# Kernel tuning notes

Hardware: AMD Instinct MI355X
Metric: run time of the kernel (lower is better)

The kernel has to match this reference:

```python
import jax, jax.numpy as jnp
import numpy as np

B, T, D_MODEL = 2, 2048, 2048
D_HEAD = 128
H_PER_G = 4
N_GROUPS = D_MODEL // (H_PER_G * D_HEAD)  # 4
ROT_BASE = 10000
EPS = 1e-6


def setup_inputs() -> dict:
    key = jax.random.key(0)
    ks = jax.random.split(key, 5)
    s = D_MODEL ** -0.5
    return {
        "x": jax.random.normal(ks[0], (B, T, D_MODEL), jnp.float32),
        "wq": jax.random.normal(ks[1], (D_MODEL, D_MODEL), jnp.float32) * s,
        "wk": jax.random.normal(ks[2], (D_MODEL, D_MODEL // H_PER_G), jnp.float32) * s,
        "wv": jax.random.normal(ks[3], (D_MODEL, D_MODEL // H_PER_G), jnp.float32) * s,
        "wo": jax.random.normal(ks[4], (D_MODEL, D_MODEL), jnp.float32) * s,
        "gq": jnp.ones((N_GROUPS, H_PER_G, D_HEAD), jnp.float32),
        "gk": jnp.ones((N_GROUPS, D_HEAD), jnp.float32),
    }


def _rmsnorm(t):
    rms = jnp.sqrt(jnp.mean(jnp.square(t), axis=-1, keepdims=True) + EPS)
    return t / rms


def _rope(t):
    # t: [..., length, width]
    length, width = t.shape[-2], t.shape[-1]
    pos = jnp.arange(length)[:, None]                       # [t,1]
    dims = jnp.arange(width // 2)[None, :]                  # [1,d/2]
    ang = jnp.power(float(ROT_BASE), -dims / (width // 2))
    rad = (pos * ang).astype(t.dtype)                       # [t,d/2]
    cos, sin = jnp.cos(rad), jnp.sin(rad)
    even, odd = jnp.split(t, 2, axis=-1)
    return jnp.concatenate([even * cos - odd * sin, even * sin + odd * cos], axis=-1)


def reference(x, wq, wk, wv, wo, gq, gk):
    b, t, _ = x.shape
    q = jnp.einsum('bti,io->bto', x, wq)
    k = jnp.einsum('bti,io->bto', x, wk)
    v = jnp.einsum('bti,io->bto', x, wv)
    # b t (g h d) -> b g h t d ; b t (g d) -> b g t d
    q = q.reshape(b, t, N_GROUPS, H_PER_G, D_HEAD).transpose(0, 2, 3, 1, 4)
    k = k.reshape(b, t, N_GROUPS, D_HEAD).transpose(0, 2, 1, 3)
    v = v.reshape(b, t, N_GROUPS, D_HEAD).transpose(0, 2, 1, 3)
    # QK RMSNorm with gains
    q = _rmsnorm(q) * gq[None, :, :, None, :]
    k = _rmsnorm(k) * gk[None, :, None, :]
    # RoPE
    q = _rope(q)
    k = _rope(k)
    mult = jnp.asarray(D_HEAD ** -0.25, x.dtype)
    s = jnp.einsum('bghid,bgjd->bghij', q * mult, k * mult)
    # causal mask: subtract 1e30 where i < j
    i = jnp.arange(t)[:, None]
    j = jnp.arange(t)[None, :]
    s = s - jnp.asarray(1e30, s.dtype) * (i < j)
    p = jax.nn.softmax(s, axis=-1)
    o = jnp.einsum('bghij,bgjd->bghid', p, v)
    o = o.transpose(0, 3, 1, 2, 4).reshape(b, t, D_MODEL)
    return jnp.einsum('bti,io->bto', o, wo)
```

## Files before the change

kernel.cpp:

```cpp
#include <hip/hip_runtime.h>
#include <cstdint>

typedef unsigned short u16;
typedef __attribute__((ext_vector_type(8))) __bf16 bf16x8;
typedef __attribute__((ext_vector_type(4))) float f32x4;
typedef __attribute__((ext_vector_type(8))) unsigned short u16x8;

#define DEV __device__ __forceinline__

DEV u16 f2bf(float f) {
  __bf16 b = (__bf16)f;
  return __builtin_bit_cast(u16, b);
}
DEV float bf2f(u16 h) { return __uint_as_float(((unsigned)h) << 16); }
DEV float exp2_fast(float x) { float r; asm("v_exp_f32 %0, %1" : "=v"(r) : "v"(x)); return r; }
DEV void barrier_mem() { asm volatile("s_barrier" ::: "memory"); }

typedef __attribute__((address_space(1))) void gvoid_t;
typedef __attribute__((address_space(3))) void lvoid_t;

DEV void gload_lds16(const void* g, void* l) {
  __builtin_amdgcn_global_load_lds((gvoid_t*)(void*)(uintptr_t)g,
                                   (lvoid_t*)l, 16, 0, 0);
}

#define B_   2
#define T_   2048
#define DM   2048
#define MROWS (B_*T_)
#define QSC  0.1275174f

__global__ void k_convert(const float* __restrict__ in, u16* __restrict__ out, int n4) {
  int i = blockIdx.x * blockDim.x + threadIdx.x;
  if (i >= n4) return;
  float4 v = ((const float4*)in)[i];
  ((ushort4*)out)[i] = make_ushort4(f2bf(v.x), f2bf(v.y), f2bf(v.z), f2bf(v.w));
}

__global__ void k_prep(const float* __restrict__ wq, const float* __restrict__ wk,
                       const float* __restrict__ wv, const float* __restrict__ wo,
                       u16* __restrict__ wqkvt, u16* __restrict__ wot,
                       float2* __restrict__ rope) {
  const int bid = blockIdx.x;
  const int tid = threadIdx.x;
  if (bid >= 10240) {
    int i = (bid - 10240) * 256 + tid;
    int pos = i >> 6, d = i & 63;
    float ang = powf(10000.0f, -(float)d / 64.0f);
    float s, c;
    sincosf((float)pos * ang, &s, &c);
    rope[i] = make_float2(c, s);
    return;
  }
  __shared__ float tile[32][33];
  const float* in;
  u16* out;
  int C, bx, by, crow0;
  if (bid < 4096)      { in = wq; out = wqkvt; C = 2048; bx = bid & 63;          by = bid >> 6;          crow0 = 0; }
  else if (bid < 5120) { in = wk; out = wqkvt; C = 512;  bx = (bid - 4096) & 15; by = (bid - 4096) >> 4; crow0 = 2048; }
  else if (bid < 6144) { in = wv; out = wqkvt; C = 512;  bx = (bid - 5120) & 15; by = (bid - 5120) >> 4; crow0 = 2560; }
  else                 { in = wo; out = wot;   C = 2048; bx = (bid - 6144) & 63; by = (bid - 6144) >> 6; crow0 = 0; }
  const int c0 = bx * 32, r0 = by * 32;
  const int tx = tid & 31, ty = tid >> 5;
  #pragma unroll
  for (int j = 0; j < 32; j += 8)
    tile[ty + j][tx] = in[(size_t)(r0 + ty + j) * C + c0 + tx];
  __syncthreads();
  #pragma unroll
  for (int j = 0; j < 32; j += 8)
    out[(size_t)(crow0 + c0 + ty + j) * 2048 + r0 + tx] = f2bf(tile[tx][ty + j]);
}

template <typename OutT>
__global__ __launch_bounds__(256) void k_gemm(
    const u16* __restrict__ A, const u16* __restrict__ BT, OutT* __restrict__ C,
    int M, int N, int K) {
  __shared__ u16 As[128 * 64];
  __shared__ u16 Bs[128 * 64];
  const int tid = threadIdx.x;
  const int w = tid >> 6, lane = tid & 63;
  const int lr = lane & 15, lg = lane >> 4;
  const int nx = gridDim.x;
  const int flat = blockIdx.y * nx + blockIdx.x;
  const int cpx = (nx * gridDim.y) >> 3;
  const int f = (flat & 7) * cpx + (flat >> 3);
  const int m0 = (f / nx) * 128, n0 = (f % nx) * 128;
  const int wr = w >> 1, wc = w & 1;
  f32x4 acc[4][4] = {};
  for (int k0 = 0; k0 < K; k0 += 64) {
    __syncthreads();
    #pragma unroll
    for (int i = 0; i < 4; i++) {
      int idx = i * 256 + tid;
      int row = idx >> 3, blk = idx & 7;
      int scol = ((blk ^ (row & 7)) << 3);
      gload_lds16(&A[(size_t)(m0 + row) * K + k0 + scol], &As[(idx & ~63) * 8]);
      gload_lds16(&BT[(size_t)(n0 + row) * K + k0 + scol], &Bs[(idx & ~63) * 8]);
    }
    __syncthreads();
    #pragma unroll
    for (int kk = 0; kk < 2; kk++) {
      bf16x8 af[4], bfr[4];
      #pragma unroll
      for (int m = 0; m < 4; m++) {
        int row = wr * 64 + m * 16 + lr;
        af[m] = *(const bf16x8*)&As[row * 64 + (((kk * 4 + lg) ^ (lr & 7)) << 3)];
      }
      #pragma unroll
      for (int n = 0; n < 4; n++) {
        int row = wc * 64 + n * 16 + lr;
        bfr[n] = *(const bf16x8*)&Bs[row * 64 + (((kk * 4 + lg) ^ (lr & 7)) << 3)];
      }
      #pragma unroll
      for (int m = 0; m < 4; m++)
        #pragma unroll
        for (int n = 0; n < 4; n++)
          acc[m][n] = __builtin_amdgcn_mfma_f32_16x16x32_bf16(af[m], bfr[n], acc[m][n], 0, 0, 0);
    }
  }
  #pragma unroll
  for (int m = 0; m < 4; m++)
    #pragma unroll
    for (int n = 0; n < 4; n++)
      #pragma unroll
      for (int r = 0; r < 4; r++) {
        int row = m0 + wr * 64 + m * 16 + lg * 4 + r;
        int col = n0 + wc * 64 + n * 16 + lr;
        if constexpr (sizeof(OutT) == 2) C[(size_t)row * N + col] = f2bf(acc[m][n][r]);
        else                             C[(size_t)row * N + col] = acc[m][n][r];
      }
}

__global__ void k_postgemm(const u16* __restrict__ qkvf, const float* __restrict__ gk,
                           const float2* __restrict__ tab, u16* __restrict__ kb,
                           u16* __restrict__ vt) {
  const int bid = blockIdx.x;
  const int w = threadIdx.x >> 6, lane = threadIdx.x & 63;
  if (bid < 4096) {
    int W = bid * 4 + w;
    int g = W & 3;
    int bt = W >> 2;
    int t = bt & 2047, b = bt >> 11;
    const u16* row = qkvf + (size_t)bt * 3072 + 2048 + (size_t)g * 128;
    float v0 = bf2f(row[lane]);
    float v1 = bf2f(row[lane + 64]);
    float ss = v0 * v0 + v1 * v1;
    #pragma unroll
    for (int off = 1; off < 64; off <<= 1) ss += __shfl_xor(ss, off, 64);
    float inv = 1.0f / sqrtf(ss * (1.0f / 128.0f) + 1e-6f);
    v0 *= inv * gk[g * 128 + lane];
    v1 *= inv * gk[g * 128 + 64 + lane];
    float2 cs = tab[t * 64 + lane];
    float o0 = v0 * cs.x - v1 * cs.y;
    float o1 = v0 * cs.y + v1 * cs.x;
    u16* orow = kb + ((size_t)((b * 4 + g) * 2048 + t)) * 128;
    orow[lane] = f2bf(o0);
    orow[lane + 64] = f2bf(o1);
  } else {
    int W = (bid - 4096) * 4 + w;
    int t8 = W & 255, dh = (W >> 8) & 1, bg = W >> 9;
    int b = bg >> 2, g = bg & 3;
    int t0 = t8 * 8;
    int d = dh * 64 + lane;
    u16x8 pack;
    #pragma unroll
    for (int j = 0; j < 8; j++)
      pack[j] = qkvf[(size_t)(b * 2048 + t0 + j) * 3072 + 2560 + g * 128 + d];
    *(u16x8*)&vt[((size_t)(bg * 128 + d)) * 2048 + t0] = pack;
  }
}

DEV void stage_tiles(const u16* kh, const u16* vh, int j0, u16* Kbuf, u16* Vbuf, int tid) {
  #pragma unroll
  for (int i = 0; i < 4; i++) {
    int idx = i * 256 + tid;
    int row = idx >> 4, blk = idx & 15;
    gload_lds16(&kh[(size_t)(j0 + row) * 128 + ((blk ^ (row & 7)) << 3)],
                &Kbuf[(idx & ~63) * 8]);
  }
  #pragma unroll
  for (int i = 0; i < 4; i++) {
    int idx = i * 256 + tid;
    int row = idx >> 3, blk = idx & 7;
    gload_lds16(&vh[(size_t)row * T_ + j0 + ((blk ^ (row & 7)) << 3)],
                &Vbuf[(idx & ~63) * 8]);
  }
}

DEV void attn_tile(const u16* __restrict__ Kc, const u16* __restrict__ Vc,
                   u16* __restrict__ Psw, const bf16x8* qf, f32x4* oacc,
                   float& lsum, int lr, int lg, int w, bool diag) {
  f32x4 s[4] = {};
  __builtin_amdgcn_s_setprio(1);
  #pragma unroll
  for (int kk = 0; kk < 4; kk++) {
    #pragma unroll
    for (int c = 0; c < 4; c++) {
      const int kvr = c * 16 + lr;
      bf16x8 kf = *(const bf16x8*)&Kc[kvr * 128 + (((kk * 4 + lg) ^ (kvr & 7)) << 3)];
      s[c] = __builtin_amdgcn_mfma_f32_16x16x32_bf16(kf, qf[kk], s[c], 0, 0, 0);
    }
  }
  __builtin_amdgcn_s_setprio(0);
  if (diag) {
    #pragma unroll
    for (int c = 0; c < 4; c++)
      #pragma unroll
      for (int r = 0; r < 4; r++)
        if (c * 16 + lg * 4 + r > w * 16 + lr) s[c][r] = -1.0e30f;
  }
  float rs = 0.f;
  #pragma unroll
  for (int c = 0; c < 4; c++)
    #pragma unroll
    for (int r = 0; r < 4; r++) {
      float pv = exp2_fast(s[c][r]);
      s[c][r] = pv;
      rs += pv;
    }
  lsum += rs;
  #pragma unroll
  for (int c = 0; c < 4; c++) {
    ushort4 q4 = make_ushort4(f2bf(s[c][0]), f2bf(s[c][1]), f2bf(s[c][2]), f2bf(s[c][3]));
    int blk8 = (c * 4 + lg) ^ ((lr & 7) << 1);
    *(ushort4*)&Psw[lr * 64 + blk8 * 4] = q4;
  }
  #pragma unroll
  for (int ks = 0; ks < 2; ks++) {
    bf16x8 pf = *(const bf16x8*)&Psw[lr * 64 +
                 (((2 * (ks * 4 + lg)) ^ ((lr & 7) << 1)) << 2)];
    __builtin_amdgcn_s_setprio(1);
    #pragma unroll
    for (int nd = 0; nd < 8; nd++) {
      const int d = nd * 16 + lr;
      bf16x8 vf = *(const bf16x8*)&Vc[d * 64 + (((ks * 4 + lg) ^ (d & 7)) << 3)];
      oacc[nd] = __builtin_amdgcn_mfma_f32_16x16x32_bf16(pf, vf, oacc[nd], 0, 0, 0);
    }
    __builtin_amdgcn_s_setprio(0);
  }
}

DEV void attn_epilogue(u16* __restrict__ ob, int b, int g, int h, int q0,
                       const f32x4* oacc, float lsum, int lr, int lg, int w) {
  lsum += __shfl_xor(lsum, 16, 64);
  lsum += __shfl_xor(lsum, 32, 64);
  float inv = 1.0f / lsum;
  float iv[4];
  #pragma unroll
  for (int r = 0; r < 4; r++) iv[r] = __shfl(inv, lg * 4 + r, 64);
  #pragma unroll
  for (int r = 0; r < 4; r++) {
    int orow = q0 + w * 16 + lg * 4 + r;
    size_t base = (size_t)(b * T_ + orow) * 2048 + (size_t)(g * 4 + h) * 128;
    #pragma unroll
    for (int nd = 0; nd < 8; nd++)
      ob[base + nd * 16 + lr] = f2bf(oacc[nd][r] * iv[r]);
  }
}

__global__ __launch_bounds__(256) void k_attn(
    const u16* __restrict__ qkvf, const float* __restrict__ gq,
    const float2* __restrict__ rope, const u16* __restrict__ kb,
    const u16* __restrict__ vtb, u16* __restrict__ ob) {
  __shared__ __align__(16) u16 Ks[2][64 * 128];
  __shared__ __align__(16) u16 Vs[2][128 * 64];
  __shared__ __align__(16) u16 Ps[4][16 * 64];
  const int bid = blockIdx.x;
  const int hg = bid & 7;
  const int rest = bid >> 3;
  const int hh = rest & 3;
  const int p = rest >> 2;
  const int b = hg >> 2, g = hg & 3, h = hh;
  const int tid = threadIdx.x;
  const int w = tid >> 6, lane = tid & 63;
  const int lr = lane & 15, lg = lane >> 4;
  const u16* kh = kb + (size_t)hg * (T_ * 128);
  const u16* vh = vtb + (size_t)hg * (128 * T_);
  const float* gqh = gq + (size_t)(g * 4 + h) * 128;

  #pragma unroll 1
  for (int half = 0; half < 2; ++half) {
    const int qblk = half ? p : 31 - p;
    const int q0 = qblk * 64;
    bf16x8 qf[4];
    {
      const int qrow = q0 + w * 16 + lr;
      const u16* qsrc = qkvf + (size_t)(b * T_ + qrow) * 3072 + (size_t)(g * 4 + h) * 128;
      float qe[4][8];
      float ss = 0.f;
      #pragma unroll
      for (int kk = 0; kk < 4; kk++) {
        u16x8 raw = *(const u16x8*)&qsrc[kk * 32 + lg * 8];
        #pragma unroll
        for (int j = 0; j < 8; j++) {
          float v = bf2f(raw[j]);
          qe[kk][j] = v;
          ss += v * v;
        }
      }
      ss += __shfl_xor(ss, 16, 64);
      ss += __shfl_xor(ss, 32, 64);
      float inv = 1.0f / sqrtf(ss * (1.0f / 128.0f) + 1e-6f);
      #pragma unroll
      for (int kk = 0; kk < 2; kk++) {
        const float2* tp = &rope[(size_t)qrow * 64 + kk * 32 + lg * 8];
        u16x8 lo, hi;
        #pragma unroll
        for (int j = 0; j < 8; j++) {
          int d = kk * 32 + lg * 8 + j;
          float v0 = qe[kk][j] * inv * gqh[d];
          float v1 = qe[kk + 2][j] * inv * gqh[d + 64];
          float2 cs = tp[j];
          lo[j] = f2bf((v0 * cs.x - v1 * cs.y) * QSC);
          hi[j] = f2bf((v0 * cs.y + v1 * cs.x) * QSC);
        }
        qf[kk] = __builtin_bit_cast(bf16x8, lo);
        qf[kk + 2] = __builtin_bit_cast(bf16x8, hi);
      }
    }

    f32x4 oacc[8] = {};
    float lsum = 0.f;

    stage_tiles(kh, vh, 0, Ks[0], Vs[0], tid);
    asm volatile("s_waitcnt vmcnt(0)" ::: "memory");
    barrier_mem();
    int cur = 0;
    for (int jt = 0; jt <= qblk; ++jt) {
      if (jt < qblk)
        stage_tiles(kh, vh, (jt + 1) * 64, Ks[cur ^ 1], Vs[cur ^ 1], tid);
      attn_tile(Ks[cur], Vs[cur], Ps[w], qf, oacc, lsum, lr, lg, w, jt == qblk);
      asm volatile("s_waitcnt vmcnt(0)" ::: "memory");
      barrier_mem();
      cur ^= 1;
    }
    attn_epilogue(ob, b, g, h, q0, oacc, lsum, lr, lg, w);
  }
}

#define OFF_XB    ((size_t)0)
#define OFF_WQKVT ((size_t)16777216)
#define OFF_WOT   ((size_t)29360128)
#define OFF_ROPE  ((size_t)37748736)
#define OFF_OB    ((size_t)38797312)
#define OFF_KB    ((size_t)55574528)
#define OFF_VTB   ((size_t)59768832)
#define OFF_QKVF  ((size_t)63963136)

extern "C" void kernel_launch(void* const* d_in, const int* in_sizes, int n_in,
                              void* d_out, int out_size, void* d_ws, size_t ws_size,
                              hipStream_t stream) {
  const float* x  = (const float*)d_in[0];
  const float* wq = (const float*)d_in[1];
  const float* wk = (const float*)d_in[2];
  const float* wv = (const float*)d_in[3];
  const float* wo = (const float*)d_in[4];
  const float* gq = (const float*)d_in[5];
  const float* gk = (const float*)d_in[6];
  float* out = (float*)d_out;
  char* ws = (char*)d_ws;

  u16*    xb    = (u16*)(ws + OFF_XB);
  u16*    wqkvt = (u16*)(ws + OFF_WQKVT);
  u16*    wot   = (u16*)(ws + OFF_WOT);
  float2* rope  = (float2*)(ws + OFF_ROPE);
  u16*    obuf  = (u16*)(ws + OFF_OB);
  u16*    kbuf  = (u16*)(ws + OFF_KB);
  u16*    vtb   = (u16*)(ws + OFF_VTB);
  u16*    qkvf  = (u16*)(ws + OFF_QKVF);

  k_convert<<<8192, 256, 0, stream>>>(x, xb, (MROWS * DM) / 4);
  k_prep<<<10752, 256, 0, stream>>>(wq, wk, wv, wo, wqkvt, wot, rope);
  k_gemm<u16><<<dim3(24, 32), 256, 0, stream>>>(xb, wqkvt, qkvf, MROWS, 3072, 2048);
  k_postgemm<<<5120, 256, 0, stream>>>(qkvf, gk, rope, kbuf, vtb);
  k_attn<<<512, 256, 0, stream>>>(qkvf, gq, rope, kbuf, vtb, obuf);
  k_gemm<float><<<dim3(16, 32), 256, 0, stream>>>(obuf, wot, out, MROWS, 2048, 2048);
}
```

Before: 199.2 us.

## Double attention query tile per block and merge input conversion into prep kernel

The attention kernel now gives each wave 32 query rows instead of 16, so a 128-row block shares every staged K/V tile across twice as many queries. The grid shrinks to 256 blocks, and each block still pairs a short and a long causal span to balance work. The separate x-to-bf16 conversion kernel is folded into k_prep to save one launch. The cost is more accumulator registers and fewer blocks, which may lower occupancy and leave compute units idle.

```diff
diff --git a/kernel.cpp b/kernel.cpp
--- a/kernel.cpp
+++ b/kernel.cpp
@@ -30,21 +30,21 @@
 #define MROWS (B_*T_)
 #define QSC  0.1275174f
 
-__global__ void k_convert(const float* __restrict__ in, u16* __restrict__ out, int n4) {
-  int i = blockIdx.x * blockDim.x + threadIdx.x;
-  if (i >= n4) return;
-  float4 v = ((const float4*)in)[i];
-  ((ushort4*)out)[i] = make_ushort4(f2bf(v.x), f2bf(v.y), f2bf(v.z), f2bf(v.w));
-}
-
-__global__ void k_prep(const float* __restrict__ wq, const float* __restrict__ wk,
+__global__ void k_prep(const float* __restrict__ x,
+                       const float* __restrict__ wq, const float* __restrict__ wk,
                        const float* __restrict__ wv, const float* __restrict__ wo,
-                       u16* __restrict__ wqkvt, u16* __restrict__ wot,
-                       float2* __restrict__ rope) {
+                       u16* __restrict__ xb, u16* __restrict__ wqkvt,
+                       u16* __restrict__ wot, float2* __restrict__ rope) {
   const int bid = blockIdx.x;
   const int tid = threadIdx.x;
-  if (bid >= 10240) {
-    int i = (bid - 10240) * 256 + tid;
+  if (bid < 8192) {
+    int i = bid * 256 + tid;
+    float4 v = ((const float4*)x)[i];
+    ((ushort4*)xb)[i] = make_ushort4(f2bf(v.x), f2bf(v.y), f2bf(v.z), f2bf(v.w));
+    return;
+  }
+  if (bid >= 18432) {
+    int i = (bid - 18432) * 256 + tid;
     int pos = i >> 6, d = i & 63;
     float ang = powf(10000.0f, -(float)d / 64.0f);
     float s, c;
@@ -53,13 +53,14 @@
     return;
   }
   __shared__ float tile[32][33];
+  const int tb = bid - 8192;
   const float* in;
   u16* out;
   int C, bx, by, crow0;
-  if (bid < 4096)      { in = wq; out = wqkvt; C = 2048; bx = bid & 63;          by = bid >> 6;          crow0 = 0; }
-  else if (bid < 5120) { in = wk; out = wqkvt; C = 512;  bx = (bid - 4096) & 15; by = (bid - 4096) >> 4; crow0 = 2048; }
-  else if (bid < 6144) { in = wv; out = wqkvt; C = 512;  bx = (bid - 5120) & 15; by = (bid - 5120) >> 4; crow0 = 2560; }
-  else                 { in = wo; out = wot;   C = 2048; bx = (bid - 6144) & 63; by = (bid - 6144) >> 6; crow0 = 0; }
+  if (tb < 4096)      { in = wq; out = wqkvt; C = 2048; bx = tb & 63;          by = tb >> 6;          crow0 = 0; }
+  else if (tb < 5120) { in = wk; out = wqkvt; C = 512;  bx = (tb - 4096) & 15; by = (tb - 4096) >> 4; crow0 = 2048; }
+  else if (tb < 6144) { in = wv; out = wqkvt; C = 512;  bx = (tb - 5120) & 15; by = (tb - 5120) >> 4; crow0 = 2560; }
+  else                { in = wo; out = wot;   C = 2048; bx = (tb - 6144) & 63; by = (tb - 6144) >> 6; crow0 = 0; }
   const int c0 = bx * 32, r0 = by * 32;
   const int tx = tid & 31, ty = tid >> 5;
   #pragma unroll
@@ -187,84 +188,13 @@
   }
 }
 
-DEV void attn_tile(const u16* __restrict__ Kc, const u16* __restrict__ Vc,
-                   u16* __restrict__ Psw, const bf16x8* qf, f32x4* oacc,
-                   float& lsum, int lr, int lg, int w, bool diag) {
-  f32x4 s[4] = {};
-  __builtin_amdgcn_s_setprio(1);
-  #pragma unroll
-  for (int kk = 0; kk < 4; kk++) {
-    #pragma unroll
-    for (int c = 0; c < 4; c++) {
-      const int kvr = c * 16 + lr;
-      bf16x8 kf = *(const bf16x8*)&Kc[kvr * 128 + (((kk * 4 + lg) ^ (kvr & 7)) << 3)];
-      s[c] = __builtin_amdgcn_mfma_f32_16x16x32_bf16(kf, qf[kk], s[c], 0, 0, 0);
-    }
-  }
-  __builtin_amdgcn_s_setprio(0);
-  if (diag) {
-    #pragma unroll
-    for (int c = 0; c < 4; c++)
-      #pragma unroll
-      for (int r = 0; r < 4; r++)
-        if (c * 16 + lg * 4 + r > w * 16 + lr) s[c][r] = -1.0e30f;
-  }
-  float rs = 0.f;
-  #pragma unroll
-  for (int c = 0; c < 4; c++)
-    #pragma unroll
-    for (int r = 0; r < 4; r++) {
-      float pv = exp2_fast(s[c][r]);
-      s[c][r] = pv;
-      rs += pv;
-    }
-  lsum += rs;
-  #pragma unroll
-  for (int c = 0; c < 4; c++) {
-    ushort4 q4 = make_ushort4(f2bf(s[c][0]), f2bf(s[c][1]), f2bf(s[c][2]), f2bf(s[c][3]));
-    int blk8 = (c * 4 + lg) ^ ((lr & 7) << 1);
-    *(ushort4*)&Psw[lr * 64 + blk8 * 4] = q4;
-  }
-  #pragma unroll
-  for (int ks = 0; ks < 2; ks++) {
-    bf16x8 pf = *(const bf16x8*)&Psw[lr * 64 +
-                 (((2 * (ks * 4 + lg)) ^ ((lr & 7) << 1)) << 2)];
-    __builtin_amdgcn_s_setprio(1);
-    #pragma unroll
-    for (int nd = 0; nd < 8; nd++) {
-      const int d = nd * 16 + lr;
-      bf16x8 vf = *(const bf16x8*)&Vc[d * 64 + (((ks * 4 + lg) ^ (d & 7)) << 3)];
-      oacc[nd] = __builtin_amdgcn_mfma_f32_16x16x32_bf16(pf, vf, oacc[nd], 0, 0, 0);
-    }
-    __builtin_amdgcn_s_setprio(0);
-  }
-}
-
-DEV void attn_epilogue(u16* __restrict__ ob, int b, int g, int h, int q0,
-                       const f32x4* oacc, float lsum, int lr, int lg, int w) {
-  lsum += __shfl_xor(lsum, 16, 64);
-  lsum += __shfl_xor(lsum, 32, 64);
-  float inv = 1.0f / lsum;
-  float iv[4];
-  #pragma unroll
-  for (int r = 0; r < 4; r++) iv[r] = __shfl(inv, lg * 4 + r, 64);
-  #pragma unroll
-  for (int r = 0; r < 4; r++) {
-    int orow = q0 + w * 16 + lg * 4 + r;
-    size_t base = (size_t)(b * T_ + orow) * 2048 + (size_t)(g * 4 + h) * 128;
-    #pragma unroll
-    for (int nd = 0; nd < 8; nd++)
-      ob[base + nd * 16 + lr] = f2bf(oacc[nd][r] * iv[r]);
-  }
-}
-
 __global__ __launch_bounds__(256) void k_attn(
     const u16* __restrict__ qkvf, const float* __restrict__ gq,
     const float2* __restrict__ rope, const u16* __restrict__ kb,
     const u16* __restrict__ vtb, u16* __restrict__ ob) {
   __shared__ __align__(16) u16 Ks[2][64 * 128];
   __shared__ __align__(16) u16 Vs[2][128 * 64];
-  __shared__ __align__(16) u16 Ps[4][16 * 64];
+  __shared__ __align__(16) u16 Ps[4][2][16 * 64];
   const int bid = blockIdx.x;
   const int hg = bid & 7;
   const int rest = bid >> 3;
@@ -280,11 +210,12 @@
 
   #pragma unroll 1
   for (int half = 0; half < 2; ++half) {
-    const int qblk = half ? p : 31 - p;
-    const int q0 = qblk * 64;
-    bf16x8 qf[4];
-    {
-      const int qrow = q0 + w * 16 + lr;
+    const int qblk = half ? p : 15 - p;
+    const int q0 = qblk * 128;
+    bf16x8 qf[2][4];
+    #pragma unroll
+    for (int t = 0; t < 2; t++) {
+      const int qrow = q0 + w * 32 + t * 16 + lr;
       const u16* qsrc = qkvf + (size_t)(b * T_ + qrow) * 3072 + (size_t)(g * 4 + h) * 128;
       float qe[4][8];
       float ss = 0.f;
@@ -314,27 +245,104 @@
           lo[j] = f2bf((v0 * cs.x - v1 * cs.y) * QSC);
           hi[j] = f2bf((v0 * cs.y + v1 * cs.x) * QSC);
         }
-        qf[kk] = __builtin_bit_cast(bf16x8, lo);
-        qf[kk + 2] = __builtin_bit_cast(bf16x8, hi);
-      }
-    }
-
-    f32x4 oacc[8] = {};
-    float lsum = 0.f;
+        qf[t][kk] = __builtin_bit_cast(bf16x8, lo);
+        qf[t][kk + 2] = __builtin_bit_cast(bf16x8, hi);
+      }
+    }
+
+    f32x4 oacc[2][8] = {};
+    float lsum[2] = {0.f, 0.f};
+    const int ntiles = 2 * qblk + 2;
 
     stage_tiles(kh, vh, 0, Ks[0], Vs[0], tid);
     asm volatile("s_waitcnt vmcnt(0)" ::: "memory");
     barrier_mem();
     int cur = 0;
-    for (int jt = 0; jt <= qblk; ++jt) {
-      if (jt < qblk)
+    for (int jt = 0; jt < ntiles; ++jt) {
+      if (jt + 1 < ntiles)
         stage_tiles(kh, vh, (jt + 1) * 64, Ks[cur ^ 1], Vs[cur ^ 1], tid);
-      attn_tile(Ks[cur], Vs[cur], Ps[w], qf, oacc, lsum, lr, lg, w, jt == qblk);
+      const u16* Kc = Ks[cur];
+      const u16* Vc = Vs[cur];
+      f32x4 s[2][4] = {};
+      __builtin_amdgcn_s_setprio(1);
+      #pragma unroll
+      for (int kk = 0; kk < 4; kk++) {
+        #pragma unroll
+        for (int c = 0; c < 4; c++) {
+          const int kvr = c * 16 + lr;
+          bf16x8 kf = *(const bf16x8*)&Kc[kvr * 128 + (((kk * 4 + lg) ^ (kvr & 7)) << 3)];
+          s[0][c] = __builtin_amdgcn_mfma_f32_16x16x32_bf16(kf, qf[0][kk], s[0][c], 0, 0, 0);
+          s[1][c] = __builtin_amdgcn_mfma_f32_16x16x32_bf16(kf, qf[1][kk], s[1][c], 0, 0, 0);
+        }
+      }
+      __builtin_amdgcn_s_setprio(0);
+      if (jt >= 2 * qblk) {
+        const int dj = jt * 64 - q0;
+        #pragma unroll
+        for (int t = 0; t < 2; t++)
+          #pragma unroll
+          for (int c = 0; c < 4; c++)
+            #pragma unroll
+            for (int r = 0; r < 4; r++)
+              if (dj + c * 16 + lg * 4 + r > w * 32 + t * 16 + lr) s[t][c][r] = -1.0e30f;
+      }
+      #pragma unroll
+      for (int t = 0; t < 2; t++) {
+        float rs = 0.f;
+        #pragma unroll
+        for (int c = 0; c < 4; c++)
+          #pragma unroll
+          for (int r = 0; r < 4; r++) {
+            float pv = exp2_fast(s[t][c][r]);
+            s[t][c][r] = pv;
+            rs += pv;
+          }
+        lsum[t] += rs;
+        #pragma unroll
+        for (int c = 0; c < 4; c++) {
+          ushort4 q4 = make_ushort4(f2bf(s[t][c][0]), f2bf(s[t][c][1]),
+                                    f2bf(s[t][c][2]), f2bf(s[t][c][3]));
+          int blk8 = (c * 4 + lg) ^ ((lr & 7) << 1);
+          *(ushort4*)&Ps[w][t][lr * 64 + blk8 * 4] = q4;
+        }
+      }
+      #pragma unroll
+      for (int ks = 0; ks < 2; ks++) {
+        const int poff = (((2 * (ks * 4 + lg)) ^ ((lr & 7) << 1)) << 2);
+        bf16x8 pf0 = *(const bf16x8*)&Ps[w][0][lr * 64 + poff];
+        bf16x8 pf1 = *(const bf16x8*)&Ps[w][1][lr * 64 + poff];
+        __builtin_amdgcn_s_setprio(1);
+        #pragma unroll
+        for (int nd = 0; nd < 8; nd++) {
+          const int d = nd * 16 + lr;
+          bf16x8 vf = *(const bf16x8*)&Vc[d * 64 + (((ks * 4 + lg) ^ (d & 7)) << 3)];
+          oacc[0][nd] = __builtin_amdgcn_mfma_f32_16x16x32_bf16(pf0, vf, oacc[0][nd], 0, 0, 0);
+          oacc[1][nd] = __builtin_amdgcn_mfma_f32_16x16x32_bf16(pf1, vf, oacc[1][nd], 0, 0, 0);
+        }
+        __builtin_amdgcn_s_setprio(0);
+      }
       asm volatile("s_waitcnt vmcnt(0)" ::: "memory");
       barrier_mem();
       cur ^= 1;
     }
-    attn_epilogue(ob, b, g, h, q0, oacc, lsum, lr, lg, w);
+    #pragma unroll
+    for (int t = 0; t < 2; t++) {
+      float ls = lsum[t];
+      ls += __shfl_xor(ls, 16, 64);
+      ls += __shfl_xor(ls, 32, 64);
+      float inv = 1.0f / ls;
+      float iv[4];
+      #pragma unroll
+      for (int r = 0; r < 4; r++) iv[r] = __shfl(inv, lg * 4 + r, 64);
+      #pragma unroll
+      for (int r = 0; r < 4; r++) {
+        int orow = q0 + w * 32 + t * 16 + lg * 4 + r;
+        size_t base = (size_t)(b * T_ + orow) * 2048 + (size_t)(g * 4 + h) * 128;
+        #pragma unroll
+        for (int nd = 0; nd < 8; nd++)
+          ob[base + nd * 16 + lr] = f2bf(oacc[t][nd][r] * iv[r]);
+      }
+    }
   }
 }
 
@@ -369,10 +377,9 @@
   u16*    vtb   = (u16*)(ws + OFF_VTB);
   u16*    qkvf  = (u16*)(ws + OFF_QKVF);
 
-  k_convert<<<8192, 256, 0, stream>>>(x, xb, (MROWS * DM) / 4);
-  k_prep<<<10752, 256, 0, stream>>>(wq, wk, wv, wo, wqkvt, wot, rope);
+  k_prep<<<18944, 256, 0, stream>>>(x, wq, wk, wv, wo, xb, wqkvt, wot, rope);
   k_gemm<u16><<<dim3(24, 32), 256, 0, stream>>>(xb, wqkvt, qkvf, MROWS, 3072, 2048);
   k_postgemm<<<5120, 256, 0, stream>>>(qkvf, gk, rope, kbuf, vtb);
-  k_attn<<<512, 256, 0, stream>>>(qkvf, gq, rope, kbuf, vtb, obuf);
+  k_attn<<<256, 256, 0, stream>>>(qkvf, gq, rope, kbuf, vtb, obuf);
   k_gemm<float><<<dim3(16, 32), 256, 0, stream>>>(obuf, wot, out, MROWS, 2048, 2048);
 }
```

Result: slower. 212.8 us (+6.8%).

## Fuse QK RMSNorm and RoPE into QKV GEMM epilogue, merge conversion kernels

Applied to the files above, without the earlier changes.

The QKV GEMM epilogue now applies RMSNorm, gains and RoPE to the Q and K tiles using LDS for the row reduction and partner-half exchange. It writes head-major Q and K buffers directly and writes V as a compact buffer for a small transpose kernel. The x conversion is folded into the weight prep kernel, and the attention kernel loads preprocessed Q instead of normalizing it. This removes the full qkvf round trip and one launch, at the cost of a heavier GEMM epilogue with extra barriers and scattered stores.

```diff
diff --git a/kernel.cpp b/kernel.cpp
--- a/kernel.cpp
+++ b/kernel.cpp
@@ -30,21 +30,21 @@
 #define MROWS (B_*T_)
 #define QSC  0.1275174f
 
-__global__ void k_convert(const float* __restrict__ in, u16* __restrict__ out, int n4) {
-  int i = blockIdx.x * blockDim.x + threadIdx.x;
-  if (i >= n4) return;
-  float4 v = ((const float4*)in)[i];
-  ((ushort4*)out)[i] = make_ushort4(f2bf(v.x), f2bf(v.y), f2bf(v.z), f2bf(v.w));
-}
-
-__global__ void k_prep(const float* __restrict__ wq, const float* __restrict__ wk,
+__global__ void k_prep(const float* __restrict__ x,
+                       const float* __restrict__ wq, const float* __restrict__ wk,
                        const float* __restrict__ wv, const float* __restrict__ wo,
-                       u16* __restrict__ wqkvt, u16* __restrict__ wot,
-                       float2* __restrict__ rope) {
+                       u16* __restrict__ xb, u16* __restrict__ wqkvt,
+                       u16* __restrict__ wot, float2* __restrict__ rope) {
   const int bid = blockIdx.x;
   const int tid = threadIdx.x;
-  if (bid >= 10240) {
-    int i = (bid - 10240) * 256 + tid;
+  if (bid < 8192) {
+    int i = bid * 256 + tid;
+    float4 v = ((const float4*)x)[i];
+    ((ushort4*)xb)[i] = make_ushort4(f2bf(v.x), f2bf(v.y), f2bf(v.z), f2bf(v.w));
+    return;
+  }
+  if (bid >= 18432) {
+    int i = (bid - 18432) * 256 + tid;
     int pos = i >> 6, d = i & 63;
     float ang = powf(10000.0f, -(float)d / 64.0f);
     float s, c;
@@ -53,13 +53,14 @@
     return;
   }
   __shared__ float tile[32][33];
+  const int tb = bid - 8192;
   const float* in;
   u16* out;
   int C, bx, by, crow0;
-  if (bid < 4096)      { in = wq; out = wqkvt; C = 2048; bx = bid & 63;          by = bid >> 6;          crow0 = 0; }
-  else if (bid < 5120) { in = wk; out = wqkvt; C = 512;  bx = (bid - 4096) & 15; by = (bid - 4096) >> 4; crow0 = 2048; }
-  else if (bid < 6144) { in = wv; out = wqkvt; C = 512;  bx = (bid - 5120) & 15; by = (bid - 5120) >> 4; crow0 = 2560; }
-  else                 { in = wo; out = wot;   C = 2048; bx = (bid - 6144) & 63; by = (bid - 6144) >> 6; crow0 = 0; }
+  if (tb < 4096)      { in = wq; out = wqkvt; C = 2048; bx = tb & 63;          by = tb >> 6;          crow0 = 0; }
+  else if (tb < 5120) { in = wk; out = wqkvt; C = 512;  bx = (tb - 4096) & 15; by = (tb - 4096) >> 4; crow0 = 2048; }
+  else if (tb < 6144) { in = wv; out = wqkvt; C = 512;  bx = (tb - 5120) & 15; by = (tb - 5120) >> 4; crow0 = 2560; }
+  else                { in = wo; out = wot;   C = 2048; bx = (tb - 6144) & 63; by = (tb - 6144) >> 6; crow0 = 0; }
   const int c0 = bx * 32, r0 = by * 32;
   const int tx = tid & 31, ty = tid >> 5;
   #pragma unroll
@@ -71,12 +72,17 @@
     out[(size_t)(crow0 + c0 + ty + j) * 2048 + r0 + tx] = f2bf(tile[tx][ty + j]);
 }
 
-template <typename OutT>
+template <int EPI, typename OutT>
 __global__ __launch_bounds__(256) void k_gemm(
     const u16* __restrict__ A, const u16* __restrict__ BT, OutT* __restrict__ C,
-    int M, int N, int K) {
-  __shared__ u16 As[128 * 64];
-  __shared__ u16 Bs[128 * 64];
+    int M, int N, int K,
+    const float* __restrict__ gq, const float* __restrict__ gk,
+    const float2* __restrict__ rope,
+    u16* __restrict__ qb, u16* __restrict__ kb, u16* __restrict__ vb) {
+  __shared__ __align__(16) u16 smem[2][128 * 64];
+  __shared__ float ssx[2][128];
+  u16* As = smem[0];
+  u16* Bs = smem[1];
   const int tid = threadIdx.x;
   const int w = tid >> 6, lane = tid & 63;
   const int lr = lane & 15, lg = lane >> 4;
@@ -118,56 +124,117 @@
           acc[m][n] = __builtin_amdgcn_mfma_f32_16x16x32_bf16(af[m], bfr[n], acc[m][n], 0, 0, 0);
     }
   }
-  #pragma unroll
-  for (int m = 0; m < 4; m++)
-    #pragma unroll
-    for (int n = 0; n < 4; n++)
-      #pragma unroll
-      for (int r = 0; r < 4; r++) {
-        int row = m0 + wr * 64 + m * 16 + lg * 4 + r;
-        int col = n0 + wc * 64 + n * 16 + lr;
-        if constexpr (sizeof(OutT) == 2) C[(size_t)row * N + col] = f2bf(acc[m][n][r]);
-        else                             C[(size_t)row * N + col] = acc[m][n][r];
+  if constexpr (EPI == 0) {
+    #pragma unroll
+    for (int m = 0; m < 4; m++)
+      #pragma unroll
+      for (int n = 0; n < 4; n++)
+        #pragma unroll
+        for (int r = 0; r < 4; r++) {
+          int row = m0 + wr * 64 + m * 16 + lg * 4 + r;
+          int col = n0 + wc * 64 + n * 16 + lr;
+          C[(size_t)row * N + col] = acc[m][n][r];
+        }
+  } else {
+    __syncthreads();
+    const int ct = n0 >> 7;
+    if (ct >= 20) {
+      #pragma unroll
+      for (int m = 0; m < 4; m++)
+        #pragma unroll
+        for (int n = 0; n < 4; n++)
+          #pragma unroll
+          for (int r = 0; r < 4; r++) {
+            int rowl = wr * 64 + m * 16 + lg * 4 + r;
+            int col = wc * 64 + n * 16 + lr;
+            vb[(size_t)(m0 + rowl) * 512 + (n0 - 2560) + col] = f2bf(acc[m][n][r]);
+          }
+    } else {
+      u16* ex = &smem[0][0];
+      float ssp[4][4];
+      #pragma unroll
+      for (int m = 0; m < 4; m++)
+        #pragma unroll
+        for (int r = 0; r < 4; r++) {
+          float s = 0.f;
+          #pragma unroll
+          for (int n = 0; n < 4; n++) { float v = acc[m][n][r]; s += v * v; }
+          ssp[m][r] = s;
+        }
+      #pragma unroll
+      for (int mask = 1; mask < 16; mask <<= 1)
+        #pragma unroll
+        for (int m = 0; m < 4; m++)
+          #pragma unroll
+          for (int r = 0; r < 4; r++)
+            ssp[m][r] += __shfl_xor(ssp[m][r], mask, 64);
+      if (lr == 0) {
+        #pragma unroll
+        for (int m = 0; m < 4; m++)
+          #pragma unroll
+          for (int r = 0; r < 4; r++)
+            ssx[wc][wr * 64 + m * 16 + lg * 4 + r] = ssp[m][r];
       }
-}
-
-__global__ void k_postgemm(const u16* __restrict__ qkvf, const float* __restrict__ gk,
-                           const float2* __restrict__ tab, u16* __restrict__ kb,
-                           u16* __restrict__ vt) {
-  const int bid = blockIdx.x;
-  const int w = threadIdx.x >> 6, lane = threadIdx.x & 63;
-  if (bid < 4096) {
-    int W = bid * 4 + w;
-    int g = W & 3;
-    int bt = W >> 2;
-    int t = bt & 2047, b = bt >> 11;
-    const u16* row = qkvf + (size_t)bt * 3072 + 2048 + (size_t)g * 128;
-    float v0 = bf2f(row[lane]);
-    float v1 = bf2f(row[lane + 64]);
-    float ss = v0 * v0 + v1 * v1;
-    #pragma unroll
-    for (int off = 1; off < 64; off <<= 1) ss += __shfl_xor(ss, off, 64);
-    float inv = 1.0f / sqrtf(ss * (1.0f / 128.0f) + 1e-6f);
-    v0 *= inv * gk[g * 128 + lane];
-    v1 *= inv * gk[g * 128 + 64 + lane];
-    float2 cs = tab[t * 64 + lane];
-    float o0 = v0 * cs.x - v1 * cs.y;
-    float o1 = v0 * cs.y + v1 * cs.x;
-    u16* orow = kb + ((size_t)((b * 4 + g) * 2048 + t)) * 128;
-    orow[lane] = f2bf(o0);
-    orow[lane + 64] = f2bf(o1);
-  } else {
-    int W = (bid - 4096) * 4 + w;
-    int t8 = W & 255, dh = (W >> 8) & 1, bg = W >> 9;
-    int b = bg >> 2, g = bg & 3;
-    int t0 = t8 * 8;
-    int d = dh * 64 + lane;
-    u16x8 pack;
-    #pragma unroll
-    for (int j = 0; j < 8; j++)
-      pack[j] = qkvf[(size_t)(b * 2048 + t0 + j) * 3072 + 2560 + g * 128 + d];
-    *(u16x8*)&vt[((size_t)(bg * 128 + d)) * 2048 + t0] = pack;
-  }
+      __syncthreads();
+      float invr[4][4];
+      #pragma unroll
+      for (int m = 0; m < 4; m++)
+        #pragma unroll
+        for (int r = 0; r < 4; r++) {
+          int rowl = wr * 64 + m * 16 + lg * 4 + r;
+          float ss = ssx[0][rowl] + ssx[1][rowl];
+          invr[m][r] = 1.0f / sqrtf(ss * (1.0f / 128.0f) + 1e-6f);
+        }
+      const bool isQ = (ct < 16);
+      const float* gain = isQ ? (gq + (size_t)ct * 128) : (gk + (size_t)(ct - 16) * 128);
+      #pragma unroll
+      for (int m = 0; m < 4; m++)
+        #pragma unroll
+        for (int n = 0; n < 4; n++)
+          #pragma unroll
+          for (int r = 0; r < 4; r++) {
+            int rowl = wr * 64 + m * 16 + lg * 4 + r;
+            int d = wc * 64 + n * 16 + lr;
+            float v = acc[m][n][r] * invr[m][r] * gain[d];
+            acc[m][n][r] = v;
+            ex[rowl * 128 + (d ^ ((rowl & 7) << 3))] = f2bf(v);
+          }
+      __syncthreads();
+      #pragma unroll
+      for (int m = 0; m < 4; m++)
+        #pragma unroll
+        for (int n = 0; n < 4; n++)
+          #pragma unroll
+          for (int r = 0; r < 4; r++) {
+            int rowl = wr * 64 + m * 16 + lg * 4 + r;
+            int d = wc * 64 + n * 16 + lr;
+            float v = acc[m][n][r];
+            float pr = bf2f(ex[rowl * 128 + ((d ^ 64) ^ ((rowl & 7) << 3))]);
+            int grow = m0 + rowl;
+            int t = grow & 2047, bI = grow >> 11;
+            float2 cs = rope[t * 64 + (d & 63)];
+            float o = (d < 64) ? (v * cs.x - pr * cs.y) : (pr * cs.y + v * cs.x);
+            if (isQ)
+              qb[((size_t)(bI * 16 + ct) * 2048 + t) * 128 + d] = f2bf(o * QSC);
+            else
+              kb[((size_t)(bI * 4 + (ct - 16)) * 2048 + t) * 128 + d] = f2bf(o);
+          }
+    }
+  }
+}
+
+__global__ void k_packvt(const u16* __restrict__ vb, u16* __restrict__ vt) {
+  int w = threadIdx.x >> 6, lane = threadIdx.x & 63;
+  int W = blockIdx.x * 4 + w;
+  int t8 = W & 255, dh = (W >> 8) & 1, bg = W >> 9;
+  int b = bg >> 2, g = bg & 3;
+  int t0 = t8 * 8;
+  int d = dh * 64 + lane;
+  u16x8 pack;
+  #pragma unroll
+  for (int j = 0; j < 8; j++)
+    pack[j] = vb[(size_t)(b * 2048 + t0 + j) * 512 + g * 128 + d];
+  *(u16x8*)&vt[((size_t)(bg * 128 + d)) * 2048 + t0] = pack;
 }
 
 DEV void stage_tiles(const u16* kh, const u16* vh, int j0, u16* Kbuf, u16* Vbuf, int tid) {
@@ -259,8 +326,7 @@
 }
 
 __global__ __launch_bounds__(256) void k_attn(
-    const u16* __restrict__ qkvf, const float* __restrict__ gq,
-    const float2* __restrict__ rope, const u16* __restrict__ kb,
+    const u16* __restrict__ qb, const u16* __restrict__ kb,
     const u16* __restrict__ vtb, u16* __restrict__ ob) {
   __shared__ __align__(16) u16 Ks[2][64 * 128];
   __shared__ __align__(16) u16 Vs[2][128 * 64];
@@ -270,54 +336,24 @@
   const int rest = bid >> 3;
   const int hh = rest & 3;
   const int p = rest >> 2;
+  const int head = hg * 4 + hh;
   const int b = hg >> 2, g = hg & 3, h = hh;
   const int tid = threadIdx.x;
   const int w = tid >> 6, lane = tid & 63;
   const int lr = lane & 15, lg = lane >> 4;
+  const u16* qh = qb + (size_t)head * (T_ * 128);
   const u16* kh = kb + (size_t)hg * (T_ * 128);
   const u16* vh = vtb + (size_t)hg * (128 * T_);
-  const float* gqh = gq + (size_t)(g * 4 + h) * 128;
 
   #pragma unroll 1
   for (int half = 0; half < 2; ++half) {
     const int qblk = half ? p : 31 - p;
     const int q0 = qblk * 64;
     bf16x8 qf[4];
-    {
-      const int qrow = q0 + w * 16 + lr;
-      const u16* qsrc = qkvf + (size_t)(b * T_ + qrow) * 3072 + (size_t)(g * 4 + h) * 128;
-      float qe[4][8];
-      float ss = 0.f;
-      #pragma unroll
-      for (int kk = 0; kk < 4; kk++) {
-        u16x8 raw = *(const u16x8*)&qsrc[kk * 32 + lg * 8];
-        #pragma unroll
-        for (int j = 0; j < 8; j++) {
-          float v = bf2f(raw[j]);
-          qe[kk][j] = v;
-          ss += v * v;
-        }
-      }
-      ss += __shfl_xor(ss, 16, 64);
-      ss += __shfl_xor(ss, 32, 64);
-      float inv = 1.0f / sqrtf(ss * (1.0f / 128.0f) + 1e-6f);
-      #pragma unroll
-      for (int kk = 0; kk < 2; kk++) {
-        const float2* tp = &rope[(size_t)qrow * 64 + kk * 32 + lg * 8];
-        u16x8 lo, hi;
-        #pragma unroll
-        for (int j = 0; j < 8; j++) {
-          int d = kk * 32 + lg * 8 + j;
-          float v0 = qe[kk][j] * inv * gqh[d];
-          float v1 = qe[kk + 2][j] * inv * gqh[d + 64];
-          float2 cs = tp[j];
-          lo[j] = f2bf((v0 * cs.x - v1 * cs.y) * QSC);
-          hi[j] = f2bf((v0 * cs.y + v1 * cs.x) * QSC);
-        }
-        qf[kk] = __builtin_bit_cast(bf16x8, lo);
-        qf[kk + 2] = __builtin_bit_cast(bf16x8, hi);
-      }
-    }
+    const int qrow = q0 + w * 16 + lr;
+    #pragma unroll
+    for (int kk = 0; kk < 4; kk++)
+      qf[kk] = *(const bf16x8*)&qh[(size_t)qrow * 128 + kk * 32 + lg * 8];
 
     f32x4 oacc[8] = {};
     float lsum = 0.f;
@@ -342,10 +378,11 @@
 #define OFF_WQKVT ((size_t)16777216)
 #define OFF_WOT   ((size_t)29360128)
 #define OFF_ROPE  ((size_t)37748736)
-#define OFF_OB    ((size_t)38797312)
+#define OFF_QB    ((size_t)38797312)
 #define OFF_KB    ((size_t)55574528)
 #define OFF_VTB   ((size_t)59768832)
-#define OFF_QKVF  ((size_t)63963136)
+#define OFF_VB    ((size_t)63963136)
+#define OFF_OB    OFF_XB
 
 extern "C" void kernel_launch(void* const* d_in, const int* in_sizes, int n_in,
                               void* d_out, int out_size, void* d_ws, size_t ws_size,
@@ -364,15 +401,18 @@
   u16*    wqkvt = (u16*)(ws + OFF_WQKVT);
   u16*    wot   = (u16*)(ws + OFF_WOT);
   float2* rope  = (float2*)(ws + OFF_ROPE);
-  u16*    obuf  = (u16*)(ws + OFF_OB);
+  u16*    qbuf  = (u16*)(ws + OFF_QB);
   u16*    kbuf  = (u16*)(ws + OFF_KB);
   u16*    vtb   = (u16*)(ws + OFF_VTB);
-  u16*    qkvf  = (u16*)(ws + OFF_QKVF);
-
-  k_convert<<<8192, 256, 0, stream>>>(x, xb, (MROWS * DM) / 4);
-  k_prep<<<10752, 256, 0, stream>>>(wq, wk, wv, wo, wqkvt, wot, rope);
-  k_gemm<u16><<<dim3(24, 32), 256, 0, stream>>>(xb, wqkvt, qkvf, MROWS, 3072, 2048);
-  k_postgemm<<<5120, 256, 0, stream>>>(qkvf, gk, rope, kbuf, vtb);
-  k_attn<<<512, 256, 0, stream>>>(qkvf, gq, rope, kbuf, vtb, obuf);
-  k_gemm<float><<<dim3(16, 32), 256, 0, stream>>>(obuf, wot, out, MROWS, 2048, 2048);
-}
+  u16*    vbuf  = (u16*)(ws + OFF_VB);
+  u16*    obuf  = (u16*)(ws + OFF_OB);
+
+  k_prep<<<18944, 256, 0, stream>>>(x, wq, wk, wv, wo, xb, wqkvt, wot, rope);
+  k_gemm<1, u16><<<dim3(24, 32), 256, 0, stream>>>(
+      xb, wqkvt, (u16*)nullptr, MROWS, 3072, 2048, gq, gk, rope, qbuf, kbuf, vbuf);
+  k_packvt<<<1024, 256, 0, stream>>>(vbuf, vtb);
+  k_attn<<<512, 256, 0, stream>>>(qbuf, kbuf, vtb, obuf);
+  k_gemm<0, float><<<dim3(16, 32), 256, 0, stream>>>(
+      obuf, wot, out, MROWS, 2048, 2048, nullptr, nullptr, nullptr,
+      nullptr, nullptr, nullptr);
+}
```

Measured after the change: 289.0 us. 1.45x slower.

## Read K/V directly from global in attention and merge convert into prep kernel

Applied to the files above, without the earlier changes.

The attention kernel no longer stages K and V tiles into double-buffered LDS with async global-to-LDS loads and barriers. Each wave now reads its K and V fragments straight from global memory (through cache) into registers for the MFMAs. Separately, the x fp32-to-bf16 conversion is folded into the weight-prep kernel, saving one launch. The attention change drops LDS traffic and block barriers but makes every wave fetch K/V itself, with four times the redundant global/L2 reads and less latency hiding.

```diff
diff --git a/kernel.cpp b/kernel.cpp
--- a/kernel.cpp
+++ b/kernel.cpp
@@ -14,7 +14,6 @@
 }
 DEV float bf2f(u16 h) { return __uint_as_float(((unsigned)h) << 16); }
 DEV float exp2_fast(float x) { float r; asm("v_exp_f32 %0, %1" : "=v"(r) : "v"(x)); return r; }
-DEV void barrier_mem() { asm volatile("s_barrier" ::: "memory"); }
 
 typedef __attribute__((address_space(1))) void gvoid_t;
 typedef __attribute__((address_space(3))) void lvoid_t;
@@ -30,21 +29,21 @@
 #define MROWS (B_*T_)
 #define QSC  0.1275174f
 
-__global__ void k_convert(const float* __restrict__ in, u16* __restrict__ out, int n4) {
-  int i = blockIdx.x * blockDim.x + threadIdx.x;
-  if (i >= n4) return;
-  float4 v = ((const float4*)in)[i];
-  ((ushort4*)out)[i] = make_ushort4(f2bf(v.x), f2bf(v.y), f2bf(v.z), f2bf(v.w));
-}
-
-__global__ void k_prep(const float* __restrict__ wq, const float* __restrict__ wk,
+__global__ void k_prep(const float* __restrict__ x,
+                       const float* __restrict__ wq, const float* __restrict__ wk,
                        const float* __restrict__ wv, const float* __restrict__ wo,
-                       u16* __restrict__ wqkvt, u16* __restrict__ wot,
-                       float2* __restrict__ rope) {
+                       u16* __restrict__ xb, u16* __restrict__ wqkvt,
+                       u16* __restrict__ wot, float2* __restrict__ rope) {
   const int bid = blockIdx.x;
   const int tid = threadIdx.x;
-  if (bid >= 10240) {
-    int i = (bid - 10240) * 256 + tid;
+  if (bid < 8192) {
+    int i = bid * 256 + tid;
+    float4 v = ((const float4*)x)[i];
+    ((ushort4*)xb)[i] = make_ushort4(f2bf(v.x), f2bf(v.y), f2bf(v.z), f2bf(v.w));
+    return;
+  }
+  if (bid >= 18432) {
+    int i = (bid - 18432) * 256 + tid;
     int pos = i >> 6, d = i & 63;
     float ang = powf(10000.0f, -(float)d / 64.0f);
     float s, c;
@@ -53,13 +52,14 @@
     return;
   }
   __shared__ float tile[32][33];
+  const int tb = bid - 8192;
   const float* in;
   u16* out;
   int C, bx, by, crow0;
-  if (bid < 4096)      { in = wq; out = wqkvt; C = 2048; bx = bid & 63;          by = bid >> 6;          crow0 = 0; }
-  else if (bid < 5120) { in = wk; out = wqkvt; C = 512;  bx = (bid - 4096) & 15; by = (bid - 4096) >> 4; crow0 = 2048; }
-  else if (bid < 6144) { in = wv; out = wqkvt; C = 512;  bx = (bid - 5120) & 15; by = (bid - 5120) >> 4; crow0 = 2560; }
-  else                 { in = wo; out = wot;   C = 2048; bx = (bid - 6144) & 63; by = (bid - 6144) >> 6; crow0 = 0; }
+  if (tb < 4096)      { in = wq; out = wqkvt; C = 2048; bx = tb & 63;          by = tb >> 6;          crow0 = 0; }
+  else if (tb < 5120) { in = wk; out = wqkvt; C = 512;  bx = (tb - 4096) & 15; by = (tb - 4096) >> 4; crow0 = 2048; }
+  else if (tb < 6144) { in = wv; out = wqkvt; C = 512;  bx = (tb - 5120) & 15; by = (tb - 5120) >> 4; crow0 = 2560; }
+  else                { in = wo; out = wot;   C = 2048; bx = (tb - 6144) & 63; by = (tb - 6144) >> 6; crow0 = 0; }
   const int c0 = bx * 32, r0 = by * 32;
   const int tx = tid & 31, ty = tid >> 5;
   #pragma unroll
@@ -170,100 +170,10 @@
   }
 }
 
-DEV void stage_tiles(const u16* kh, const u16* vh, int j0, u16* Kbuf, u16* Vbuf, int tid) {
-  #pragma unroll
-  for (int i = 0; i < 4; i++) {
-    int idx = i * 256 + tid;
-    int row = idx >> 4, blk = idx & 15;
-    gload_lds16(&kh[(size_t)(j0 + row) * 128 + ((blk ^ (row & 7)) << 3)],
-                &Kbuf[(idx & ~63) * 8]);
-  }
-  #pragma unroll
-  for (int i = 0; i < 4; i++) {
-    int idx = i * 256 + tid;
-    int row = idx >> 3, blk = idx & 7;
-    gload_lds16(&vh[(size_t)row * T_ + j0 + ((blk ^ (row & 7)) << 3)],
-                &Vbuf[(idx & ~63) * 8]);
-  }
-}
-
-DEV void attn_tile(const u16* __restrict__ Kc, const u16* __restrict__ Vc,
-                   u16* __restrict__ Psw, const bf16x8* qf, f32x4* oacc,
-                   float& lsum, int lr, int lg, int w, bool diag) {
-  f32x4 s[4] = {};
-  __builtin_amdgcn_s_setprio(1);
-  #pragma unroll
-  for (int kk = 0; kk < 4; kk++) {
-    #pragma unroll
-    for (int c = 0; c < 4; c++) {
-      const int kvr = c * 16 + lr;
-      bf16x8 kf = *(const bf16x8*)&Kc[kvr * 128 + (((kk * 4 + lg) ^ (kvr & 7)) << 3)];
-      s[c] = __builtin_amdgcn_mfma_f32_16x16x32_bf16(kf, qf[kk], s[c], 0, 0, 0);
-    }
-  }
-  __builtin_amdgcn_s_setprio(0);
-  if (diag) {
-    #pragma unroll
-    for (int c = 0; c < 4; c++)
-      #pragma unroll
-      for (int r = 0; r < 4; r++)
-        if (c * 16 + lg * 4 + r > w * 16 + lr) s[c][r] = -1.0e30f;
-  }
-  float rs = 0.f;
-  #pragma unroll
-  for (int c = 0; c < 4; c++)
-    #pragma unroll
-    for (int r = 0; r < 4; r++) {
-      float pv = exp2_fast(s[c][r]);
-      s[c][r] = pv;
-      rs += pv;
-    }
-  lsum += rs;
-  #pragma unroll
-  for (int c = 0; c < 4; c++) {
-    ushort4 q4 = make_ushort4(f2bf(s[c][0]), f2bf(s[c][1]), f2bf(s[c][2]), f2bf(s[c][3]));
-    int blk8 = (c * 4 + lg) ^ ((lr & 7) << 1);
-    *(ushort4*)&Psw[lr * 64 + blk8 * 4] = q4;
-  }
-  #pragma unroll
-  for (int ks = 0; ks < 2; ks++) {
-    bf16x8 pf = *(const bf16x8*)&Psw[lr * 64 +
-                 (((2 * (ks * 4 + lg)) ^ ((lr & 7) << 1)) << 2)];
-    __builtin_amdgcn_s_setprio(1);
-    #pragma unroll
-    for (int nd = 0; nd < 8; nd++) {
-      const int d = nd * 16 + lr;
-      bf16x8 vf = *(const bf16x8*)&Vc[d * 64 + (((ks * 4 + lg) ^ (d & 7)) << 3)];
-      oacc[nd] = __builtin_amdgcn_mfma_f32_16x16x32_bf16(pf, vf, oacc[nd], 0, 0, 0);
-    }
-    __builtin_amdgcn_s_setprio(0);
-  }
-}
-
-DEV void attn_epilogue(u16* __restrict__ ob, int b, int g, int h, int q0,
-                       const f32x4* oacc, float lsum, int lr, int lg, int w) {
-  lsum += __shfl_xor(lsum, 16, 64);
-  lsum += __shfl_xor(lsum, 32, 64);
-  float inv = 1.0f / lsum;
-  float iv[4];
-  #pragma unroll
-  for (int r = 0; r < 4; r++) iv[r] = __shfl(inv, lg * 4 + r, 64);
-  #pragma unroll
-  for (int r = 0; r < 4; r++) {
-    int orow = q0 + w * 16 + lg * 4 + r;
-    size_t base = (size_t)(b * T_ + orow) * 2048 + (size_t)(g * 4 + h) * 128;
-    #pragma unroll
-    for (int nd = 0; nd < 8; nd++)
-      ob[base + nd * 16 + lr] = f2bf(oacc[nd][r] * iv[r]);
-  }
-}
-
 __global__ __launch_bounds__(256) void k_attn(
     const u16* __restrict__ qkvf, const float* __restrict__ gq,
     const float2* __restrict__ rope, const u16* __restrict__ kb,
     const u16* __restrict__ vtb, u16* __restrict__ ob) {
-  __shared__ __align__(16) u16 Ks[2][64 * 128];
-  __shared__ __align__(16) u16 Vs[2][128 * 64];
   __shared__ __align__(16) u16 Ps[4][16 * 64];
   const int bid = blockIdx.x;
   const int hg = bid & 7;
@@ -322,19 +232,76 @@
     f32x4 oacc[8] = {};
     float lsum = 0.f;
 
-    stage_tiles(kh, vh, 0, Ks[0], Vs[0], tid);
-    asm volatile("s_waitcnt vmcnt(0)" ::: "memory");
-    barrier_mem();
-    int cur = 0;
     for (int jt = 0; jt <= qblk; ++jt) {
-      if (jt < qblk)
-        stage_tiles(kh, vh, (jt + 1) * 64, Ks[cur ^ 1], Vs[cur ^ 1], tid);
-      attn_tile(Ks[cur], Vs[cur], Ps[w], qf, oacc, lsum, lr, lg, w, jt == qblk);
-      asm volatile("s_waitcnt vmcnt(0)" ::: "memory");
-      barrier_mem();
-      cur ^= 1;
-    }
-    attn_epilogue(ob, b, g, h, q0, oacc, lsum, lr, lg, w);
+      const int j0 = jt * 64;
+      f32x4 s[4] = {};
+      __builtin_amdgcn_s_setprio(1);
+      #pragma unroll
+      for (int c = 0; c < 4; c++) {
+        const u16* krow = &kh[(size_t)(j0 + c * 16 + lr) * 128 + lg * 8];
+        bf16x8 kf0 = *(const bf16x8*)&krow[0];
+        bf16x8 kf1 = *(const bf16x8*)&krow[32];
+        bf16x8 kf2 = *(const bf16x8*)&krow[64];
+        bf16x8 kf3 = *(const bf16x8*)&krow[96];
+        s[c] = __builtin_amdgcn_mfma_f32_16x16x32_bf16(kf0, qf[0], s[c], 0, 0, 0);
+        s[c] = __builtin_amdgcn_mfma_f32_16x16x32_bf16(kf1, qf[1], s[c], 0, 0, 0);
+        s[c] = __builtin_amdgcn_mfma_f32_16x16x32_bf16(kf2, qf[2], s[c], 0, 0, 0);
+        s[c] = __builtin_amdgcn_mfma_f32_16x16x32_bf16(kf3, qf[3], s[c], 0, 0, 0);
+      }
+      __builtin_amdgcn_s_setprio(0);
+      if (jt == qblk) {
+        #pragma unroll
+        for (int c = 0; c < 4; c++)
+          #pragma unroll
+          for (int r = 0; r < 4; r++)
+            if (c * 16 + lg * 4 + r > w * 16 + lr) s[c][r] = -1.0e30f;
+      }
+      float rs = 0.f;
+      #pragma unroll
+      for (int c = 0; c < 4; c++)
+        #pragma unroll
+        for (int r = 0; r < 4; r++) {
+          float pv = exp2_fast(s[c][r]);
+          s[c][r] = pv;
+          rs += pv;
+        }
+      lsum += rs;
+      #pragma unroll
+      for (int c = 0; c < 4; c++) {
+        ushort4 q4 = make_ushort4(f2bf(s[c][0]), f2bf(s[c][1]), f2bf(s[c][2]), f2bf(s[c][3]));
+        int blk8 = (c * 4 + lg) ^ ((lr & 7) << 1);
+        *(ushort4*)&Ps[w][lr * 64 + blk8 * 4] = q4;
+      }
+      #pragma unroll
+      for (int ks = 0; ks < 2; ks++) {
+        bf16x8 pf = *(const bf16x8*)&Ps[w][lr * 64 +
+                     (((2 * (ks * 4 + lg)) ^ ((lr & 7) << 1)) << 2)];
+        __builtin_amdgcn_s_setprio(1);
+        #pragma unroll
+        for (int nd = 0; nd < 8; nd++) {
+          bf16x8 vf = *(const bf16x8*)&vh[(size_t)(nd * 16 + lr) * 2048 + j0 + (ks * 4 + lg) * 8];
+          oacc[nd] = __builtin_amdgcn_mfma_f32_16x16x32_bf16(pf, vf, oacc[nd], 0, 0, 0);
+        }
+        __builtin_amdgcn_s_setprio(0);
+      }
+    }
+    {
+      float ls = lsum;
+      ls += __shfl_xor(ls, 16, 64);
+      ls += __shfl_xor(ls, 32, 64);
+      float inv = 1.0f / ls;
+      float iv[4];
+      #pragma unroll
+      for (int r = 0; r < 4; r++) iv[r] = __shfl(inv, lg * 4 + r, 64);
+      #pragma unroll
+      for (int r = 0; r < 4; r++) {
+        int orow = q0 + w * 16 + lg * 4 + r;
+        size_t base = (size_t)(b * T_ + orow) * 2048 + (size_t)(g * 4 + h) * 128;
+        #pragma unroll
+        for (int nd = 0; nd < 8; nd++)
+          ob[base + nd * 16 + lr] = f2bf(oacc[nd][r] * iv[r]);
+      }
+    }
   }
 }
 
@@ -369,8 +336,7 @@
   u16*    vtb   = (u16*)(ws + OFF_VTB);
   u16*    qkvf  = (u16*)(ws + OFF_QKVF);
 
-  k_convert<<<8192, 256, 0, stream>>>(x, xb, (MROWS * DM) / 4);
-  k_prep<<<10752, 256, 0, stream>>>(wq, wk, wv, wo, wqkvt, wot, rope);
+  k_prep<<<18944, 256, 0, stream>>>(x, wq, wk, wv, wo, xb, wqkvt, wot, rope);
   k_gemm<u16><<<dim3(24, 32), 256, 0, stream>>>(xb, wqkvt, qkvf, MROWS, 3072, 2048);
   k_postgemm<<<5120, 256, 0, stream>>>(qkvf, gk, rope, kbuf, vtb);
   k_attn<<<512, 256, 0, stream>>>(qkvf, gq, rope, kbuf, vtb, obuf);
```

New measurement: 376.9 us. 1.89x slower.
